# Performance work log

Hardware: AMD Instinct MI355X
Metric: run time of the kernel (lower is better)

## Reference

```python
import jax, jax.numpy as jnp
import numpy as np

N_EMBD = 1024
N_HEAD = 16
HEAD_DIM = N_EMBD // N_HEAD


def setup_inputs() -> dict:
    key = jax.random.key(0)
    ks = jax.random.split(key, 9)
    B, T, C = 4, 2048, N_EMBD
    s = 1.0 / np.sqrt(C)
    return {
        "x": jax.random.normal(ks[0], (B, T, C), dtype=jnp.float32),
        "Wk": jax.random.normal(ks[1], (C, C), dtype=jnp.float32) * s,
        "bk": jax.random.normal(ks[2], (C,), dtype=jnp.float32) * 0.02,
        "Wq": jax.random.normal(ks[3], (C, C), dtype=jnp.float32) * s,
        "bq": jax.random.normal(ks[4], (C,), dtype=jnp.float32) * 0.02,
        "Wv": jax.random.normal(ks[5], (C, C), dtype=jnp.float32) * s,
        "bv": jax.random.normal(ks[6], (C,), dtype=jnp.float32) * 0.02,
        "Wp": jax.random.normal(ks[7], (C, C), dtype=jnp.float32) * s,
        "bp": jax.random.normal(ks[8], (C,), dtype=jnp.float32) * 0.02,
    }


def reference(x, Wk, bk, Wq, bq, Wv, bv, Wp, bp):
    B, T, C = x.shape
    nh, hs = N_HEAD, HEAD_DIM
    # linear projections; weights stored as [in, out] (x @ W + b)
    k = (x @ Wk + bk).reshape(B, T, nh, hs).transpose(0, 2, 1, 3)  # [B,nh,T,hs]
    q = (x @ Wq + bq).reshape(B, T, nh, hs).transpose(0, 2, 1, 3)
    v = (x @ Wv + bv).reshape(B, T, nh, hs).transpose(0, 2, 1, 3)
    att = jnp.einsum("bhqd,bhkd->bhqk", q, k) / jnp.sqrt(jnp.float32(hs))
    causal = jnp.tril(jnp.ones((T, T), dtype=bool))  # [T,T]
    att = jnp.where(causal[None, None], att, -jnp.inf)
    att = jax.nn.softmax(att, axis=-1)
    y = jnp.einsum("bhqk,bhkd->bhqd", att, v)  # [B,nh,T,hs]
    y = y.transpose(0, 2, 1, 3).reshape(B, T, C)
    return y @ Wp + bp
```

## Files before the change

kernel.cpp:

```cpp
#include <hip/hip_runtime.h>

#define TSEQ 2048
#define CDIM 1024
#define NH 16
#define HS 64
#define BATCH 4

typedef __attribute__((ext_vector_type(8))) short short8;
typedef __attribute__((ext_vector_type(4))) short s16x4;
typedef __attribute__((ext_vector_type(4))) float f32x4;

__device__ __forceinline__ short f2bf(float f) {
    unsigned u = __builtin_bit_cast(unsigned, f);
    unsigned r = (u + 0x7fffu + ((u >> 16) & 1u)) >> 16;
    return (short)r;
}

__device__ __forceinline__ void gload_lds16(const void* g, void* l) {
    __builtin_amdgcn_global_load_lds((const __attribute__((address_space(1))) void*)g,
                                     (__attribute__((address_space(3))) void*)l, 16, 0, 0);
}

#define FENCE() asm volatile("" ::: "memory")

__global__ void cvt_x(const float* __restrict__ x, short* __restrict__ o, int n4) {
    int i = blockIdx.x * 256 + threadIdx.x;
    if (i >= n4) return;
    float4 v = ((const float4*)x)[i];
    s16x4 r;
    r[0] = f2bf(v.x); r[1] = f2bf(v.y); r[2] = f2bf(v.z); r[3] = f2bf(v.w);
    ((s16x4*)o)[i] = r;
}

__global__ void wtrans(const float* __restrict__ Wk, const float* __restrict__ Wq,
                       const float* __restrict__ Wv, const float* __restrict__ Wp,
                       short* __restrict__ Wcat, short* __restrict__ Wpt) {
    const float* src; short* dst;
    if (blockIdx.z == 0)      { src = Wq; dst = Wcat; }
    else if (blockIdx.z == 1) { src = Wk; dst = Wcat + 1048576; }
    else if (blockIdx.z == 2) { src = Wv; dst = Wcat + 2097152; }
    else                      { src = Wp; dst = Wpt; }
    __shared__ float tl[64][65];
    int tx = threadIdx.x & 63, ty = threadIdx.x >> 6;
    int k0 = blockIdx.x * 64, n0 = blockIdx.y * 64;
#pragma unroll
    for (int i = 0; i < 16; ++i) {
        int r = i * 4 + ty;
        tl[r][tx] = src[(size_t)(k0 + r) * CDIM + n0 + tx];
    }
    __syncthreads();
#pragma unroll
    for (int i = 0; i < 16; ++i) {
        int r = i * 4 + ty;
        dst[(size_t)(n0 + r) * CDIM + k0 + tx] = f2bf(tl[tx][r]);
    }
}

__global__ __launch_bounds__(512, 4) void gemm96(const short* __restrict__ A,
                                                 const short* __restrict__ Bt,
                                                 const float* __restrict__ bq,
                                                 const float* __restrict__ bk,
                                                 const float* __restrict__ bv,
                                                 float alphaQ,
                                                 short* __restrict__ C,
                                                 short* __restrict__ Vt) {
    __shared__ short As[256 * 64];
    __shared__ short Bs[96 * 64];
    const int t = threadIdx.x;
    const int lane = t & 63, w = t >> 6;
    const int lr = lane & 15, lg = lane >> 4;
    const int wr = w >> 1, wc = w & 1;
    const int tl = (blockIdx.x & 7) * 128 + (blockIdx.x >> 3);
    const int mbase = (tl >> 5) * 256, nbase = (tl & 31) * 96;
    f32x4 acc[4][3] = {};
    for (int k0 = 0; k0 < 1024; k0 += 64) {
#pragma unroll
        for (int i = 0; i < 4; ++i) {
            int chunk = i * 512 + t;
            int r = chunk >> 3, c = chunk & 7;
            int cl = c ^ (r & 7);
            gload_lds16(A + (size_t)(mbase + r) * 1024 + k0 + cl * 8, As + chunk * 8);
        }
        {
            int r = t >> 3, c = t & 7;
            int cl = c ^ (r & 7);
            gload_lds16(Bt + (size_t)(nbase + r) * 1024 + k0 + cl * 8, Bs + t * 8);
            if (t < 256) {
                int chunk = 512 + t;
                int r2 = chunk >> 3, c2 = chunk & 7;
                int cl2 = c2 ^ (r2 & 7);
                gload_lds16(Bt + (size_t)(nbase + r2) * 1024 + k0 + cl2 * 8, Bs + chunk * 8);
            }
        }
        __syncthreads();
#pragma unroll
        for (int ks = 0; ks < 2; ++ks) {
            short8 a[4], b[3];
#pragma unroll
            for (int mi = 0; mi < 4; ++mi) {
                int row = wr * 64 + mi * 16 + lr;
                int ch = (ks * 4 + lg) ^ (row & 7);
                a[mi] = *(const short8*)(As + row * 64 + ch * 8);
            }
#pragma unroll
            for (int ni = 0; ni < 3; ++ni) {
                int row = wc * 48 + ni * 16 + lr;
                int ch = (ks * 4 + lg) ^ (row & 7);
                b[ni] = *(const short8*)(Bs + row * 64 + ch * 8);
            }
#pragma unroll
            for (int mi = 0; mi < 4; ++mi)
#pragma unroll
                for (int ni = 0; ni < 3; ++ni)
                    acc[mi][ni] = __builtin_amdgcn_mfma_f32_16x16x32_bf16(a[mi], b[ni],
                                                                          acc[mi][ni], 0, 0, 0);
        }
        __syncthreads();
    }
    const int btok = mbase & (TSEQ - 1);
    const int bidx = mbase >> 11;
#pragma unroll
    for (int mi = 0; mi < 4; ++mi) {
#pragma unroll
        for (int ni = 0; ni < 3; ++ni) {
            const int col = nbase + wc * 48 + ni * 16 + lr;
            const float bvv = (col < 1024) ? bq[col]
                            : (col < 2048) ? bk[col - 1024] : bv[col - 2048];
            if (col >= 2048) {
                const int dfull = col - 2048;
                const int tok0 = btok + wr * 64 + mi * 16 + lg * 4;
                s16x4 pk;
#pragma unroll
                for (int ii = 0; ii < 4; ++ii) pk[ii] = f2bf(acc[mi][ni][ii] + bvv);
                *(s16x4*)(Vt + (size_t)(bidx * 1024 + dfull) * TSEQ + tok0) = pk;
            } else {
                const float alpha = (col < 1024) ? alphaQ : 1.0f;
#pragma unroll
                for (int ii = 0; ii < 4; ++ii) {
                    const int row = mbase + wr * 64 + mi * 16 + lg * 4 + ii;
                    C[(size_t)row * 3072 + col] = f2bf((acc[mi][ni][ii] + bvv) * alpha);
                }
            }
        }
    }
}

__global__ __launch_bounds__(256) void gemm_bt(const short* __restrict__ A,
                                               const short* __restrict__ Bt,
                                               const float* __restrict__ bias,
                                               float* __restrict__ Cout) {
    __shared__ short As[128 * 64];
    __shared__ short Bs[128 * 64];
    const int t = threadIdx.x;
    const int lane = t & 63, w = t >> 6;
    const int lr = lane & 15, lg = lane >> 4;
    const int wr = w >> 1, wc = w & 1;
    const int mbase = blockIdx.y * 128, nbase = blockIdx.x * 128;
    f32x4 acc[4][4] = {};
    for (int k0 = 0; k0 < 1024; k0 += 64) {
#pragma unroll
        for (int i = 0; i < 4; ++i) {
            int chunk = i * 256 + t;
            int r = chunk >> 3, c = chunk & 7;
            int cl = c ^ (r & 7);
            gload_lds16(A + (size_t)(mbase + r) * 1024 + k0 + cl * 8, As + chunk * 8);
            gload_lds16(Bt + (size_t)(nbase + r) * 1024 + k0 + cl * 8, Bs + chunk * 8);
        }
        __syncthreads();
#pragma unroll
        for (int ks = 0; ks < 2; ++ks) {
            short8 a[4], b[4];
#pragma unroll
            for (int mi = 0; mi < 4; ++mi) {
                int row = wr * 64 + mi * 16 + lr;
                int ch = (ks * 4 + lg) ^ (row & 7);
                a[mi] = *(const short8*)(As + row * 64 + ch * 8);
            }
#pragma unroll
            for (int ni = 0; ni < 4; ++ni) {
                int row = wc * 64 + ni * 16 + lr;
                int ch = (ks * 4 + lg) ^ (row & 7);
                b[ni] = *(const short8*)(Bs + row * 64 + ch * 8);
            }
#pragma unroll
            for (int mi = 0; mi < 4; ++mi)
#pragma unroll
                for (int ni = 0; ni < 4; ++ni)
                    acc[mi][ni] = __builtin_amdgcn_mfma_f32_16x16x32_bf16(a[mi], b[ni],
                                                                          acc[mi][ni], 0, 0, 0);
        }
        __syncthreads();
    }
#pragma unroll
    for (int mi = 0; mi < 4; ++mi) {
#pragma unroll
        for (int ni = 0; ni < 4; ++ni) {
            int col = nbase + wc * 64 + ni * 16 + lr;
            float bvv = bias[col];
#pragma unroll
            for (int i = 0; i < 4; ++i) {
                int row = mbase + wr * 64 + mi * 16 + lg * 4 + i;
                Cout[(size_t)row * 1024 + col] = acc[mi][ni][i] + bvv;
            }
        }
    }
}

__global__ __launch_bounds__(256, 4) void attn(const short* __restrict__ QKV,
                                               const short* __restrict__ Vt,
                                               short* __restrict__ Y) {
    __shared__ short Kl[2][64 * 64];
    __shared__ short Vl[2][64 * 64];
    __shared__ short Pl[4][16 * 64];
    const int t = threadIdx.x, lane = t & 63, w = t >> 6;
    const int lr = lane & 15, lg = lane >> 4;
    const int bid = blockIdx.x;
    const int cx = bid & 7, sx = bid >> 3;
    const int bh = cx * 8 + (sx >> 4), pb = sx & 15;
    const int b = bh >> 4, h = bh & 15;
    const size_t rowbase = (size_t)b * TSEQ;
    const float SHIFT2 = 17.31234049f;
    const int sr = t >> 3, sc = t & 7, scl = sc ^ (sr & 7);
    const short* Kg = QKV + 1024 + h * HS;

#define STAGE(bf, j0n) do { \
    gload_lds16(Kg + (rowbase + (j0n) + sr) * 3072 + scl * 8, &Kl[bf][t * 8]); \
    gload_lds16(Kg + (rowbase + (j0n) + 32 + sr) * 3072 + scl * 8, &Kl[bf][(256 + t) * 8]); \
    gload_lds16(Vt + (size_t)(bh * 64 + sr) * TSEQ + (j0n) + scl * 8, &Vl[bf][t * 8]); \
    gload_lds16(Vt + (size_t)(bh * 64 + 32 + sr) * TSEQ + (j0n) + scl * 8, \
                &Vl[bf][(256 + t) * 8]); \
} while (0)

    const int useg0 = 31 - pb, useg1 = pb;
    for (int sg = 0; sg < 2; ++sg) {
        const int u = sg ? useg1 : useg0;
        const int q0w = u * 64 + w * 16;
        const int niter = u + 1;
        short8 qf[2];
#pragma unroll
        for (int ks = 0; ks < 2; ++ks)
            qf[ks] = *(const short8*)(QKV + (rowbase + q0w + lr) * 3072 + h * HS +
                                      ks * 32 + lg * 8);
        float l_i[4] = {0.f, 0.f, 0.f, 0.f};
        f32x4 o[4] = {};
        STAGE(0, 0);
        int buf = 0;
        for (int jt = 0; jt < niter; ++jt) {
            const int j0 = jt * 64;
            if (jt + 1 < niter) {
                STAGE(buf ^ 1, j0 + 64);
                asm volatile("s_waitcnt vmcnt(4)" ::: "memory");
            } else {
                asm volatile("s_waitcnt vmcnt(0)" ::: "memory");
            }
            __builtin_amdgcn_s_barrier();
            FENCE();
            f32x4 s[4];
            __builtin_amdgcn_s_setprio(1);
#pragma unroll
            for (int nt = 0; nt < 4; ++nt) {
                s[nt] = f32x4{0.f, 0.f, 0.f, 0.f};
#pragma unroll
                for (int ks = 0; ks < 2; ++ks) {
                    short8 kf = *(const short8*)(&Kl[buf][(nt * 16 + lr) * 64 +
                                                          (((ks * 4 + lg) ^ (lr & 7)) * 8)]);
                    s[nt] = __builtin_amdgcn_mfma_f32_16x16x32_bf16(qf[ks], kf, s[nt], 0, 0, 0);
                }
            }
            __builtin_amdgcn_s_setprio(0);
            if (jt == niter - 1) {
#pragma unroll
                for (int nt = 0; nt < 4; ++nt)
#pragma unroll
                    for (int i = 0; i < 4; ++i) {
                        int kv = j0 + nt * 16 + lr;
                        int q = q0w + lg * 4 + i;
                        if (kv > q) s[nt][i] = -__builtin_inff();
                    }
            }
#pragma unroll
            for (int i = 0; i < 4; ++i) {
                const int ql = lg * 4 + i;
                float pt[4];
#pragma unroll
                for (int nt = 0; nt < 4; ++nt) {
                    float p = __builtin_amdgcn_exp2f(s[nt][i] - SHIFT2);
                    unsigned uu = __builtin_bit_cast(unsigned, p);
                    int chv = ((nt * 2 + (lr >> 3)) ^ (ql & 7));
                    Pl[w][ql * 64 + chv * 8 + (lr & 7)] = (short)(uu >> 16);
                    pt[nt] = __builtin_bit_cast(float, uu & 0xffff0000u);
                }
                l_i[i] += (pt[0] + pt[1]) + (pt[2] + pt[3]);
            }
            short8 pf[2];
#pragma unroll
            for (int ks = 0; ks < 2; ++ks)
                pf[ks] = *(const short8*)(&Pl[w][lr * 64 + (((ks * 4 + lg) ^ (lr & 7)) * 8)]);
            __builtin_amdgcn_s_setprio(1);
#pragma unroll
            for (int nd = 0; nd < 4; ++nd)
#pragma unroll
                for (int ks = 0; ks < 2; ++ks) {
                    short8 vf = *(const short8*)(&Vl[buf][(nd * 16 + lr) * 64 +
                                                          (((ks * 4 + lg) ^ (lr & 7)) * 8)]);
                    o[nd] = __builtin_amdgcn_mfma_f32_16x16x32_bf16(pf[ks], vf, o[nd], 0, 0, 0);
                }
            __builtin_amdgcn_s_setprio(0);
            FENCE();
            __builtin_amdgcn_s_barrier();
            buf ^= 1;
        }
#pragma unroll
        for (int i = 0; i < 4; ++i) {
            float l = l_i[i];
            l += __shfl_xor(l, 1);
            l += __shfl_xor(l, 2);
            l += __shfl_xor(l, 4);
            l += __shfl_xor(l, 8);
            float inv = 1.0f / l;
            int q = q0w + lg * 4 + i;
#pragma unroll
            for (int nd = 0; nd < 4; ++nd)
                Y[(rowbase + q) * 1024 + h * HS + nd * 16 + lr] = f2bf(o[nd][i] * inv);
        }
        __syncthreads();
    }
#undef STAGE
}

extern "C" void kernel_launch(void* const* d_in, const int* in_sizes, int n_in,
                              void* d_out, int out_size, void* d_ws, size_t ws_size,
                              hipStream_t stream) {
    const float* x  = (const float*)d_in[0];
    const float* Wk = (const float*)d_in[1];
    const float* bk = (const float*)d_in[2];
    const float* Wq = (const float*)d_in[3];
    const float* bq = (const float*)d_in[4];
    const float* Wv = (const float*)d_in[5];
    const float* bv = (const float*)d_in[6];
    const float* Wp = (const float*)d_in[7];
    const float* bp = (const float*)d_in[8];
    float* out = (float*)d_out;
    char* ws = (char*)d_ws;
    const size_t MB = 1024 * 1024;
    short* xb   = (short*)(ws);
    short* Wcat = (short*)(ws + 16 * MB);
    short* Wpt  = (short*)(ws + 22 * MB);
    short* QKVb = (short*)(ws + 24 * MB);
    short* Yb   = xb;
    short* VtT  = (short*)d_out;

    const float alphaQ = 0.125f * 1.44269504088896f;

    cvt_x<<<8192, 256, 0, stream>>>(x, xb, 2097152);
    wtrans<<<dim3(16, 16, 4), 256, 0, stream>>>(Wk, Wq, Wv, Wp, Wcat, Wpt);
    gemm96<<<1024, 512, 0, stream>>>(xb, Wcat, bq, bk, bv, alphaQ, QKVb, VtT);
    attn<<<1024, 256, 0, stream>>>(QKVb, VtT, Yb);
    gemm_bt<<<dim3(8, 64), 256, 0, stream>>>(Yb, Wpt, bp, out);
}
```

Measured before the change: 165.6 us.

## Merge prep kernels and use 128-row query tiles in attention with causal skip

```diff
diff --git a/kernel.cpp b/kernel.cpp
--- a/kernel.cpp
+++ b/kernel.cpp
@@ -23,26 +23,29 @@
 
 #define FENCE() asm volatile("" ::: "memory")
 
-__global__ void cvt_x(const float* __restrict__ x, short* __restrict__ o, int n4) {
-    int i = blockIdx.x * 256 + threadIdx.x;
-    if (i >= n4) return;
-    float4 v = ((const float4*)x)[i];
-    s16x4 r;
-    r[0] = f2bf(v.x); r[1] = f2bf(v.y); r[2] = f2bf(v.z); r[3] = f2bf(v.w);
-    ((s16x4*)o)[i] = r;
-}
-
-__global__ void wtrans(const float* __restrict__ Wk, const float* __restrict__ Wq,
-                       const float* __restrict__ Wv, const float* __restrict__ Wp,
-                       short* __restrict__ Wcat, short* __restrict__ Wpt) {
+__global__ void prep(const float* __restrict__ x, short* __restrict__ xb,
+                     const float* __restrict__ Wk, const float* __restrict__ Wq,
+                     const float* __restrict__ Wv, const float* __restrict__ Wp,
+                     short* __restrict__ Wcat, short* __restrict__ Wpt) {
+    __shared__ float tl[64][65];
+    const int bid = blockIdx.x, t = threadIdx.x;
+    if (bid < 8192) {
+        int i = bid * 256 + t;
+        float4 v = ((const float4*)x)[i];
+        s16x4 r;
+        r[0] = f2bf(v.x); r[1] = f2bf(v.y); r[2] = f2bf(v.z); r[3] = f2bf(v.w);
+        ((s16x4*)xb)[i] = r;
+        return;
+    }
+    const int widx = bid - 8192;
+    const int z = widx >> 8, rem = widx & 255;
+    const int k0 = (rem & 15) * 64, n0 = (rem >> 4) * 64;
     const float* src; short* dst;
-    if (blockIdx.z == 0)      { src = Wq; dst = Wcat; }
-    else if (blockIdx.z == 1) { src = Wk; dst = Wcat + 1048576; }
-    else if (blockIdx.z == 2) { src = Wv; dst = Wcat + 2097152; }
-    else                      { src = Wp; dst = Wpt; }
-    __shared__ float tl[64][65];
-    int tx = threadIdx.x & 63, ty = threadIdx.x >> 6;
-    int k0 = blockIdx.x * 64, n0 = blockIdx.y * 64;
+    if (z == 0)      { src = Wq; dst = Wcat; }
+    else if (z == 1) { src = Wk; dst = Wcat + 1048576; }
+    else if (z == 2) { src = Wv; dst = Wcat + 2097152; }
+    else             { src = Wp; dst = Wpt; }
+    const int tx = t & 63, ty = t >> 6;
 #pragma unroll
     for (int i = 0; i < 16; ++i) {
         int r = i * 4 + ty;
@@ -206,17 +209,17 @@
     }
 }
 
-__global__ __launch_bounds__(256, 4) void attn(const short* __restrict__ QKV,
+__global__ __launch_bounds__(512, 3) void attn(const short* __restrict__ QKV,
                                                const short* __restrict__ Vt,
                                                short* __restrict__ Y) {
     __shared__ short Kl[2][64 * 64];
     __shared__ short Vl[2][64 * 64];
-    __shared__ short Pl[4][16 * 64];
+    __shared__ short Pl[8][16 * 64];
     const int t = threadIdx.x, lane = t & 63, w = t >> 6;
     const int lr = lane & 15, lg = lane >> 4;
     const int bid = blockIdx.x;
     const int cx = bid & 7, sx = bid >> 3;
-    const int bh = cx * 8 + (sx >> 4), pb = sx & 15;
+    const int bh = cx * 8 + (sx >> 3), pb = sx & 7;
     const int b = bh >> 4, h = bh & 15;
     const size_t rowbase = (size_t)b * TSEQ;
     const float SHIFT2 = 17.31234049f;
@@ -225,17 +228,14 @@
 
 #define STAGE(bf, j0n) do { \
     gload_lds16(Kg + (rowbase + (j0n) + sr) * 3072 + scl * 8, &Kl[bf][t * 8]); \
-    gload_lds16(Kg + (rowbase + (j0n) + 32 + sr) * 3072 + scl * 8, &Kl[bf][(256 + t) * 8]); \
     gload_lds16(Vt + (size_t)(bh * 64 + sr) * TSEQ + (j0n) + scl * 8, &Vl[bf][t * 8]); \
-    gload_lds16(Vt + (size_t)(bh * 64 + 32 + sr) * TSEQ + (j0n) + scl * 8, \
-                &Vl[bf][(256 + t) * 8]); \
 } while (0)
 
-    const int useg0 = 31 - pb, useg1 = pb;
+    const int useg0 = 15 - pb, useg1 = pb;
     for (int sg = 0; sg < 2; ++sg) {
         const int u = sg ? useg1 : useg0;
-        const int q0w = u * 64 + w * 16;
-        const int niter = u + 1;
+        const int q0w = u * 128 + w * 16;
+        const int niter = 2 * u + 2;
         short8 qf[2];
 #pragma unroll
         for (int ks = 0; ks < 2; ++ks)
@@ -249,63 +249,70 @@
             const int j0 = jt * 64;
             if (jt + 1 < niter) {
                 STAGE(buf ^ 1, j0 + 64);
-                asm volatile("s_waitcnt vmcnt(4)" ::: "memory");
+                asm volatile("s_waitcnt vmcnt(2)" ::: "memory");
             } else {
                 asm volatile("s_waitcnt vmcnt(0)" ::: "memory");
             }
             __builtin_amdgcn_s_barrier();
             FENCE();
-            f32x4 s[4];
-            __builtin_amdgcn_s_setprio(1);
-#pragma unroll
-            for (int nt = 0; nt < 4; ++nt) {
-                s[nt] = f32x4{0.f, 0.f, 0.f, 0.f};
-#pragma unroll
-                for (int ks = 0; ks < 2; ++ks) {
-                    short8 kf = *(const short8*)(&Kl[buf][(nt * 16 + lr) * 64 +
-                                                          (((ks * 4 + lg) ^ (lr & 7)) * 8)]);
-                    s[nt] = __builtin_amdgcn_mfma_f32_16x16x32_bf16(qf[ks], kf, s[nt], 0, 0, 0);
+            if (j0 <= q0w + 15) {
+                f32x4 s[4];
+                __builtin_amdgcn_s_setprio(1);
+#pragma unroll
+                for (int nt = 0; nt < 4; ++nt) {
+                    s[nt] = f32x4{0.f, 0.f, 0.f, 0.f};
+                    if (j0 + nt * 16 <= q0w + 15) {
+#pragma unroll
+                        for (int ks = 0; ks < 2; ++ks) {
+                            short8 kf = *(const short8*)(&Kl[buf][(nt * 16 + lr) * 64 +
+                                                        (((ks * 4 + lg) ^ (lr & 7)) * 8)]);
+                            s[nt] = __builtin_amdgcn_mfma_f32_16x16x32_bf16(qf[ks], kf,
+                                                                            s[nt], 0, 0, 0);
+                        }
+                    }
                 }
-            }
-            __builtin_amdgcn_s_setprio(0);
-            if (jt == niter - 1) {
-#pragma unroll
-                for (int nt = 0; nt < 4; ++nt)
-#pragma unroll
-                    for (int i = 0; i < 4; ++i) {
-                        int kv = j0 + nt * 16 + lr;
-                        int q = q0w + lg * 4 + i;
-                        if (kv > q) s[nt][i] = -__builtin_inff();
+                __builtin_amdgcn_s_setprio(0);
+                if (j0 + 63 > q0w) {
+#pragma unroll
+                    for (int nt = 0; nt < 4; ++nt)
+#pragma unroll
+                        for (int i = 0; i < 4; ++i) {
+                            int kv = j0 + nt * 16 + lr;
+                            int q = q0w + lg * 4 + i;
+                            if (kv > q) s[nt][i] = -__builtin_inff();
+                        }
+                }
+#pragma unroll
+                for (int i = 0; i < 4; ++i) {
+                    const int ql = lg * 4 + i;
+                    float pt[4];
+#pragma unroll
+                    for (int nt = 0; nt < 4; ++nt) {
+                        float p = __builtin_amdgcn_exp2f(s[nt][i] - SHIFT2);
+                        unsigned uu = __builtin_bit_cast(unsigned, p);
+                        int chv = ((nt * 2 + (lr >> 3)) ^ (ql & 7));
+                        Pl[w][ql * 64 + chv * 8 + (lr & 7)] = (short)(uu >> 16);
+                        pt[nt] = __builtin_bit_cast(float, uu & 0xffff0000u);
                     }
-            }
-#pragma unroll
-            for (int i = 0; i < 4; ++i) {
-                const int ql = lg * 4 + i;
-                float pt[4];
-#pragma unroll
-                for (int nt = 0; nt < 4; ++nt) {
-                    float p = __builtin_amdgcn_exp2f(s[nt][i] - SHIFT2);
-                    unsigned uu = __builtin_bit_cast(unsigned, p);
-                    int chv = ((nt * 2 + (lr >> 3)) ^ (ql & 7));
-                    Pl[w][ql * 64 + chv * 8 + (lr & 7)] = (short)(uu >> 16);
-                    pt[nt] = __builtin_bit_cast(float, uu & 0xffff0000u);
+                    l_i[i] += (pt[0] + pt[1]) + (pt[2] + pt[3]);
                 }
-                l_i[i] += (pt[0] + pt[1]) + (pt[2] + pt[3]);
-            }
-            short8 pf[2];
-#pragma unroll
-            for (int ks = 0; ks < 2; ++ks)
-                pf[ks] = *(const short8*)(&Pl[w][lr * 64 + (((ks * 4 + lg) ^ (lr & 7)) * 8)]);
-            __builtin_amdgcn_s_setprio(1);
-#pragma unroll
-            for (int nd = 0; nd < 4; ++nd)
-#pragma unroll
-                for (int ks = 0; ks < 2; ++ks) {
-                    short8 vf = *(const short8*)(&Vl[buf][(nd * 16 + lr) * 64 +
-                                                          (((ks * 4 + lg) ^ (lr & 7)) * 8)]);
-                    o[nd] = __builtin_amdgcn_mfma_f32_16x16x32_bf16(pf[ks], vf, o[nd], 0, 0, 0);
-                }
-            __builtin_amdgcn_s_setprio(0);
+                short8 pf[2];
+#pragma unroll
+                for (int ks = 0; ks < 2; ++ks)
+                    pf[ks] = *(const short8*)(&Pl[w][lr * 64 +
+                                                     (((ks * 4 + lg) ^ (lr & 7)) * 8)]);
+                __builtin_amdgcn_s_setprio(1);
+#pragma unroll
+                for (int nd = 0; nd < 4; ++nd)
+#pragma unroll
+                    for (int ks = 0; ks < 2; ++ks) {
+                        short8 vf = *(const short8*)(&Vl[buf][(nd * 16 + lr) * 64 +
+                                                    (((ks * 4 + lg) ^ (lr & 7)) * 8)]);
+                        o[nd] = __builtin_amdgcn_mfma_f32_16x16x32_bf16(pf[ks], vf,
+                                                                        o[nd], 0, 0, 0);
+                    }
+                __builtin_amdgcn_s_setprio(0);
+            }
             FENCE();
             __builtin_amdgcn_s_barrier();
             buf ^= 1;
@@ -352,9 +359,8 @@
 
     const float alphaQ = 0.125f * 1.44269504088896f;
 
-    cvt_x<<<8192, 256, 0, stream>>>(x, xb, 2097152);
-    wtrans<<<dim3(16, 16, 4), 256, 0, stream>>>(Wk, Wq, Wv, Wp, Wcat, Wpt);
+    prep<<<9216, 256, 0, stream>>>(x, xb, Wk, Wq, Wv, Wp, Wcat, Wpt);
     gemm96<<<1024, 512, 0, stream>>>(xb, Wcat, bq, bk, bv, alphaQ, QKVb, VtT);
-    attn<<<1024, 256, 0, stream>>>(QKVb, VtT, Yb);
+    attn<<<512, 512, 0, stream>>>(QKVb, VtT, Yb);
     gemm_bt<<<dim3(8, 64), 256, 0, stream>>>(Yb, Wpt, bp, out);
 }
```

Measured after the change: 163.3 us, median of 2. Within noise of the previous version (-1.4%).
